# Performance work log

Hardware: AMD Instinct MI355X
Metric: run time of the kernel (lower is better)

Reference implementation:

```python
import jax, jax.numpy as jnp
import numpy as np

N = 5_000_000   # total nodes
B = 16384       # number of graphs
F_X = 4
F_U = 1


def setup_inputs() -> dict:
    key = jax.random.key(0)
    k = jax.random.split(key, 6)
    x = jax.random.normal(k[0], (N, F_X), dtype=jnp.float32)
    batch = jnp.sort(jax.random.randint(k[1], (N,), 0, B)).astype(jnp.int64)
    u = jax.random.normal(k[2], (B, F_U), dtype=jnp.float32)
    d = F_U + F_X  # 5
    W1 = jax.random.normal(k[3], (d, d), dtype=jnp.float32) / np.sqrt(d)
    b1 = jnp.zeros((d,), dtype=jnp.float32)
    W2 = jax.random.normal(k[4], (d, F_U), dtype=jnp.float32) / np.sqrt(d)
    b2 = jnp.zeros((F_U,), dtype=jnp.float32)
    return {"x": x, "batch": batch, "u": u, "W1": W1, "b1": b1, "W2": W2, "b2": b2}


def reference(x, batch, u, W1, b1, W2, b2):
    # scatter_mean(x, batch, dim=0): segment sum / segment count (empty -> 0)
    seg_sum = jax.ops.segment_sum(x, batch, num_segments=B)            # [B, F_x]
    cnt = jax.ops.segment_sum(jnp.ones((x.shape[0],), x.dtype), batch,
                              num_segments=B)                          # [B]
    mean = jnp.where(cnt[:, None] > 0, seg_sum / jnp.maximum(cnt, 1.0)[:, None], 0.0)
    h = jnp.concatenate([u, mean], axis=1)                             # [B, 5]
    h = jax.nn.leaky_relu(h @ W1 + b1, negative_slope=0.1)
    return h @ W2 + b2                                                 # [B, 1]
```

## Files before the change

### kernel.cpp

```cpp
#include <hip/hip_runtime.h>

#define WAVE 64

__global__ void __launch_bounds__(256)
fused_seg_mean_mlp(const float4* __restrict__ x,
                   const int* __restrict__ batch,
                   const float* __restrict__ u,
                   const float* __restrict__ W1,
                   const float* __restrict__ b1,
                   const float* __restrict__ W2,
                   const float* __restrict__ b2,
                   float* __restrict__ out,
                   int N, int B) {
    const int wid  = (blockIdx.x * blockDim.x + threadIdx.x) >> 6;
    const int lane = threadIdx.x & (WAVE - 1);
    if (wid >= B) return;

    const int t = wid + (lane & 1);
    int lo = 0, hi = N;
    while (lo < hi) {
        const int mid = (lo + hi) >> 1;
        if (batch[mid] < t) lo = mid + 1;
        else                hi = mid;
    }
    const int start = __shfl(lo, 0);
    const int end   = __shfl(lo, 1);

    float4 a0 = make_float4(0.f, 0.f, 0.f, 0.f);
    float4 a1 = make_float4(0.f, 0.f, 0.f, 0.f);
    float4 a2 = make_float4(0.f, 0.f, 0.f, 0.f);
    float4 a3 = make_float4(0.f, 0.f, 0.f, 0.f);

    int i = start + lane;
    for (; i + 3 * WAVE < end; i += 4 * WAVE) {
        float4 v0 = x[i];
        float4 v1 = x[i + WAVE];
        float4 v2 = x[i + 2 * WAVE];
        float4 v3 = x[i + 3 * WAVE];
        a0.x += v0.x; a0.y += v0.y; a0.z += v0.z; a0.w += v0.w;
        a1.x += v1.x; a1.y += v1.y; a1.z += v1.z; a1.w += v1.w;
        a2.x += v2.x; a2.y += v2.y; a2.z += v2.z; a2.w += v2.w;
        a3.x += v3.x; a3.y += v3.y; a3.z += v3.z; a3.w += v3.w;
    }
    for (; i < end; i += WAVE) {
        float4 v = x[i];
        a0.x += v.x; a0.y += v.y; a0.z += v.z; a0.w += v.w;
    }

    a0.x += a1.x; a0.y += a1.y; a0.z += a1.z; a0.w += a1.w;
    a2.x += a3.x; a2.y += a3.y; a2.z += a3.z; a2.w += a3.w;
    a0.x += a2.x; a0.y += a2.y; a0.z += a2.z; a0.w += a2.w;

    #pragma unroll
    for (int off = 32; off > 0; off >>= 1) {
        a0.x += __shfl_down(a0.x, off);
        a0.y += __shfl_down(a0.y, off);
        a0.z += __shfl_down(a0.z, off);
        a0.w += __shfl_down(a0.w, off);
    }

    if (lane == 0) {
        const int cnt = end - start;
        const float inv = (cnt > 0) ? (1.0f / (float)cnt) : 0.0f;

        float h[5];
        h[0] = u[wid];
        h[1] = a0.x * inv;
        h[2] = a0.y * inv;
        h[3] = a0.z * inv;
        h[4] = a0.w * inv;

        float o = b2[0];
        #pragma unroll
        for (int j = 0; j < 5; ++j) {
            float s = b1[j];
            #pragma unroll
            for (int i2 = 0; i2 < 5; ++i2) s += h[i2] * W1[i2 * 5 + j];
            s = (s > 0.0f) ? s : 0.1f * s;
            o += s * W2[j];
        }
        out[wid] = o;
    }
}

extern "C" void kernel_launch(void* const* d_in, const int* in_sizes, int n_in,
                              void* d_out, int out_size, void* d_ws, size_t ws_size,
                              hipStream_t stream) {
    const float* x     = (const float*)d_in[0];
    const int*   batch = (const int*)  d_in[1];
    const float* u     = (const float*)d_in[2];
    const float* W1    = (const float*)d_in[3];
    const float* b1    = (const float*)d_in[4];
    const float* W2    = (const float*)d_in[5];
    const float* b2    = (const float*)d_in[6];
    float* out = (float*)d_out;

    const int N = in_sizes[0] / 4;
    const int B = out_size;

    (void)d_ws; (void)ws_size;

    const int threads = 256;
    const int blocks  = (int)(((long long)B * WAVE + threads - 1) / threads);
    fused_seg_mean_mlp<<<blocks, threads, 0, stream>>>(
        (const float4*)x, batch, u, W1, b1, W2, b2, out, N, B);
}
```

Measured before the change: 149.3 us.

## Replace per-segment binary search with grid-stride segmented scan and atomics

Instead of one wave per graph doing a binary search and a reduction, the work is split into three kernels. The first zeroes a workspace accumulator, the second streams x and batch in fixed chunks of 64 elements and combines runs of the same segment with a shuffle-based segmented scan. Each segment run's tail lane then atomically adds its partial sums and count to the accumulator, and a separate MLP kernel finishes the computation. This removes the binary-search latency and the load imbalance across segments, at the cost of two extra launches, atomic traffic, reading batch fully, and a non-deterministic summation order.

```diff
diff --git a/kernel.cpp b/kernel.cpp
--- a/kernel.cpp
+++ b/kernel.cpp
@@ -2,85 +2,97 @@
 
 #define WAVE 64
 
+typedef float v4f __attribute__((ext_vector_type(4)));
+
+__global__ void zero_acc_kernel(float* __restrict__ acc, int n) {
+    const int i = blockIdx.x * blockDim.x + threadIdx.x;
+    if (i < n) acc[i] = 0.0f;
+}
+
 __global__ void __launch_bounds__(256)
-fused_seg_mean_mlp(const float4* __restrict__ x,
-                   const int* __restrict__ batch,
-                   const float* __restrict__ u,
-                   const float* __restrict__ W1,
-                   const float* __restrict__ b1,
-                   const float* __restrict__ W2,
-                   const float* __restrict__ b2,
-                   float* __restrict__ out,
-                   int N, int B) {
-    const int wid  = (blockIdx.x * blockDim.x + threadIdx.x) >> 6;
-    const int lane = threadIdx.x & (WAVE - 1);
-    if (wid >= B) return;
+partial_sums_kernel(const v4f* __restrict__ x,
+                    const int* __restrict__ batch,
+                    float* __restrict__ acc,
+                    int N) {
+    const int nwaves = (gridDim.x * blockDim.x) >> 6;
+    const int gwave  = (blockIdx.x * blockDim.x + threadIdx.x) >> 6;
+    const int lane   = threadIdx.x & (WAVE - 1);
+    const int nchunks = (N + WAVE - 1) >> 6;
 
-    const int t = wid + (lane & 1);
-    int lo = 0, hi = N;
-    while (lo < hi) {
-        const int mid = (lo + hi) >> 1;
-        if (batch[mid] < t) lo = mid + 1;
-        else                hi = mid;
+    for (int c = gwave; c < nchunks; c += nwaves) {
+        const int i = (c << 6) + lane;
+        v4f v = (v4f)(0.0f);
+        int seg = -1;
+        if (i < N) {
+            v   = __builtin_nontemporal_load(&x[i]);
+            seg = __builtin_nontemporal_load(&batch[i]);
+        }
+
+        #pragma unroll
+        for (int off = 1; off < WAVE; off <<= 1) {
+            float ox = __shfl_up(v.x, off);
+            float oy = __shfl_up(v.y, off);
+            float oz = __shfl_up(v.z, off);
+            float ow = __shfl_up(v.w, off);
+            int   os = __shfl_up(seg, off);
+            if (lane >= off && os == seg) {
+                v.x += ox; v.y += oy; v.z += oz; v.w += ow;
+            }
+        }
+
+        const int nseg = __shfl_down(seg, 1);
+        const bool last = (lane == WAVE - 1) || (nseg != seg);
+
+        const int pseg = __shfl_up(seg, 1);
+        const bool head = (lane == 0) || (pseg != seg);
+        const unsigned long long hmask = __ballot(head);
+
+        if (last && seg >= 0) {
+            const unsigned long long below = hmask & ((2ULL << lane) - 1ULL);
+            const int startl = 63 - __clzll(below);
+            const float cnt = (float)(lane - startl + 1);
+            float* a = acc + (long long)seg * 5;
+            atomicAdd(a + 0, v.x);
+            atomicAdd(a + 1, v.y);
+            atomicAdd(a + 2, v.z);
+            atomicAdd(a + 3, v.w);
+            atomicAdd(a + 4, cnt);
+        }
     }
-    const int start = __shfl(lo, 0);
-    const int end   = __shfl(lo, 1);
+}
 
-    float4 a0 = make_float4(0.f, 0.f, 0.f, 0.f);
-    float4 a1 = make_float4(0.f, 0.f, 0.f, 0.f);
-    float4 a2 = make_float4(0.f, 0.f, 0.f, 0.f);
-    float4 a3 = make_float4(0.f, 0.f, 0.f, 0.f);
+__global__ void __launch_bounds__(256)
+mlp_kernel(const float* __restrict__ acc,
+           const float* __restrict__ u,
+           const float* __restrict__ W1,
+           const float* __restrict__ b1,
+           const float* __restrict__ W2,
+           const float* __restrict__ b2,
+           float* __restrict__ out, int B) {
+    const int s = blockIdx.x * blockDim.x + threadIdx.x;
+    if (s >= B) return;
 
-    int i = start + lane;
-    for (; i + 3 * WAVE < end; i += 4 * WAVE) {
-        float4 v0 = x[i];
-        float4 v1 = x[i + WAVE];
-        float4 v2 = x[i + 2 * WAVE];
-        float4 v3 = x[i + 3 * WAVE];
-        a0.x += v0.x; a0.y += v0.y; a0.z += v0.z; a0.w += v0.w;
-        a1.x += v1.x; a1.y += v1.y; a1.z += v1.z; a1.w += v1.w;
-        a2.x += v2.x; a2.y += v2.y; a2.z += v2.z; a2.w += v2.w;
-        a3.x += v3.x; a3.y += v3.y; a3.z += v3.z; a3.w += v3.w;
+    const float* a = acc + (long long)s * 5;
+    const float cnt = a[4];
+    const float inv = (cnt > 0.0f) ? (1.0f / cnt) : 0.0f;
+
+    float h[5];
+    h[0] = u[s];
+    h[1] = a[0] * inv;
+    h[2] = a[1] * inv;
+    h[3] = a[2] * inv;
+    h[4] = a[3] * inv;
+
+    float o = b2[0];
+    #pragma unroll
+    for (int j = 0; j < 5; ++j) {
+        float t = b1[j];
+        #pragma unroll
+        for (int i2 = 0; i2 < 5; ++i2) t += h[i2] * W1[i2 * 5 + j];
+        t = (t > 0.0f) ? t : 0.1f * t;
+        o += t * W2[j];
     }
-    for (; i < end; i += WAVE) {
-        float4 v = x[i];
-        a0.x += v.x; a0.y += v.y; a0.z += v.z; a0.w += v.w;
-    }
-
-    a0.x += a1.x; a0.y += a1.y; a0.z += a1.z; a0.w += a1.w;
-    a2.x += a3.x; a2.y += a3.y; a2.z += a3.z; a2.w += a3.w;
-    a0.x += a2.x; a0.y += a2.y; a0.z += a2.z; a0.w += a2.w;
-
-    #pragma unroll
-    for (int off = 32; off > 0; off >>= 1) {
-        a0.x += __shfl_down(a0.x, off);
-        a0.y += __shfl_down(a0.y, off);
-        a0.z += __shfl_down(a0.z, off);
-        a0.w += __shfl_down(a0.w, off);
-    }
-
-    if (lane == 0) {
-        const int cnt = end - start;
-        const float inv = (cnt > 0) ? (1.0f / (float)cnt) : 0.0f;
-
-        float h[5];
-        h[0] = u[wid];
-        h[1] = a0.x * inv;
-        h[2] = a0.y * inv;
-        h[3] = a0.z * inv;
-        h[4] = a0.w * inv;
-
-        float o = b2[0];
-        #pragma unroll
-        for (int j = 0; j < 5; ++j) {
-            float s = b1[j];
-            #pragma unroll
-            for (int i2 = 0; i2 < 5; ++i2) s += h[i2] * W1[i2 * 5 + j];
-            s = (s > 0.0f) ? s : 0.1f * s;
-            o += s * W2[j];
-        }
-        out[wid] = o;
-    }
+    out[s] = o;
 }
 
 extern "C" void kernel_launch(void* const* d_in, const int* in_sizes, int n_in,
@@ -98,10 +110,14 @@
     const int N = in_sizes[0] / 4;
     const int B = out_size;
 
-    (void)d_ws; (void)ws_size;
+    float* acc = (float*)d_ws;
+    const int accN = B * 5;
 
-    const int threads = 256;
-    const int blocks  = (int)(((long long)B * WAVE + threads - 1) / threads);
-    fused_seg_mean_mlp<<<blocks, threads, 0, stream>>>(
-        (const float4*)x, batch, u, W1, b1, W2, b2, out, N, B);
+    zero_acc_kernel<<<(accN + 255) / 256, 256, 0, stream>>>(acc, accN);
+
+    partial_sums_kernel<<<2048, 256, 0, stream>>>(
+        (const v4f*)x, batch, acc, N);
+
+    mlp_kernel<<<(B + 255) / 256, 256, 0, stream>>>(
+        acc, u, W1, b1, W2, b2, out, B);
 }
```

After: 163.9 us. +9.8%, slower.
